# Kernel tuning notes

Measured on AMD Instinct MI355X. Metric: run time of the kernel, lower is better.

The kernel has to match this reference:

```python
import jax, jax.numpy as jnp
import numpy as np

# batch, net nodes/graph, vnr nodes/graph, hidden, static feats, vnr feats, vnf types, value out
B, NN, NV, H, FS, FV, T, O = 64, 1000, 10, 128, 8, 6, 8, 64
EN, EV = B * NN * 8, B * NV * 4  # total edges (avg degree 8 / 4)


def _gat(h, src, dst, W, al, ar, b):
    """dgl GATConv, num_heads=1, activation=None, allow_zero_in_degree=True."""
    n = h.shape[0]
    z = h @ W                                                    # [N,H]
    e = jax.nn.leaky_relu((z @ al)[src] + (z @ ar)[dst], 0.2)    # [E]
    emax = jax.ops.segment_max(e, dst, num_segments=n)
    ee = jnp.exp(e - emax[dst])
    alpha = ee / jax.ops.segment_sum(ee, dst, num_segments=n)[dst]
    return jax.ops.segment_sum(z[src] * alpha[:, None], dst, num_segments=n) + b


def _gru_cell(x, h, W_ih, W_hh, b_ih, b_hh):
    gi = x @ W_ih.T + b_ih
    gh = h @ W_hh.T + b_hh
    ir, iz, in_ = jnp.split(gi, 3, axis=-1)
    hr, hz, hn = jnp.split(gh, 3, axis=-1)
    r = jax.nn.sigmoid(ir + hr)
    z = jax.nn.sigmoid(iz + hz)
    n = jnp.tanh(in_ + r * hn)
    return (1.0 - z) * n + z * h


def _forward(static_feat, vnr_feat, nmask,
             Ws1, als1, ars1, bs1, Ws2, als2, ars2, bs2, Ws3, als3, ars3, bs3,
             Wv1, alv1, arv1, bv1, Wv2, alv2, arv2, bv2, Wv3, alv3, arv3, bv3,
             W_attn, v_attn, W_ih, W_hh, b_ih, b_hh, h0, W_out, b_out,
             src_s, dst_s, src_v, dst_v, vnr_VNF, net_VNF):
    # ---- graph encoders: 3 stacked GAT layers each ----
    hs = _gat(static_feat, src_s, dst_s, Ws1, als1, ars1, bs1)
    hs = _gat(hs, src_s, dst_s, Ws2, als2, ars2, bs2)
    hs = _gat(hs, src_s, dst_s, Ws3, als3, ars3, bs3)            # [B*NN,H]
    hv = _gat(vnr_feat, src_v, dst_v, Wv1, alv1, arv1, bv1)
    hv = _gat(hv, src_v, dst_v, Wv2, alv2, arv2, bv2)
    hv = _gat(hv, src_v, dst_v, Wv3, alv3, arv3, bv3)            # [B*NV,H]
    static_hidden = hs.reshape(B, NN, H).transpose(0, 2, 1)      # [B,H,NN]
    vnr_hidden = hv.reshape(B, NV, H).transpose(0, 2, 1)         # [B,H,NV]

    # ---- pointer decoder ----
    netV = net_VNF.reshape(B, NN, T)
    # mask[b,i,n] = netV[b, n, vnr_VNF[b,i]]
    masks = jnp.take_along_axis(netV[:, None, :, :], vnr_VNF[:, :, None, None], axis=3)[..., 0]  # [B,NV,NN]

    def step(h, x):
        h_new = _gru_cell(x, h, W_ih, W_hh, b_ih, b_hh)          # [B,H]
        cat = jnp.concatenate(
            [static_hidden, jnp.broadcast_to(h_new[:, :, None], (B, H, NN))], axis=1)  # [B,2H,NN]
        attn = jnp.einsum('h,bhn->bn', v_attn,
                          jnp.tanh(jnp.einsum('hk,bkn->bhn', W_attn, cat)))
        return h_new, attn

    h0b = jnp.broadcast_to(h0, (B, H))
    xs = vnr_hidden.transpose(2, 0, 1)                            # [NV,B,H]
    _, attns = jax.lax.scan(step, h0b, xs)                        # [NV,B,NN]
    pi = (attns.transpose(1, 0, 2) + jnp.log(masks.astype(jnp.float32))).reshape(B, -1)

    # ---- value head ----
    nm = nmask.reshape(B, NV)
    y1 = (vnr_hidden.transpose(0, 2, 1) * nm[:, :, None]).sum(1) / nm.sum(1, keepdims=True)
    y2 = static_hidden.mean(2)
    val = jnp.concatenate([y1, y2], axis=1) @ W_out.T + b_out     # [B,O]
    return pi, val


def setup_inputs() -> dict:
    key = jax.random.key(0)
    ks = iter(jax.random.split(key, 60))

    def nrm(shape, fan):
        return jax.random.normal(next(ks), shape, jnp.float32) / np.sqrt(fan).astype(np.float32)

    inp = {
        'static_feat': jax.random.normal(next(ks), (B * NN, FS), jnp.float32),
        'vnr_feat': jax.random.normal(next(ks), (B * NV, FV), jnp.float32),
        'nmask': jnp.ones((B * NV,), jnp.float32),
    }
    for pfx, fin in (('s1', FS), ('s2', H), ('s3', H), ('v1', FV), ('v2', H), ('v3', H)):
        inp['W' + pfx] = nrm((fin, H), fin)
        inp['al' + pfx] = nrm((H,), H)
        inp['ar' + pfx] = nrm((H,), H)
        inp['b' + pfx] = jnp.zeros((H,), jnp.float32)
    inp['W_attn'] = nrm((H, 2 * H), 2 * H)
    inp['v_attn'] = nrm((H,), H)
    inp['W_ih'] = nrm((3 * H, H), H)
    inp['W_hh'] = nrm((3 * H, H), H)
    inp['b_ih'] = jnp.zeros((3 * H,), jnp.float32)
    inp['b_hh'] = jnp.zeros((3 * H,), jnp.float32)
    inp['h0'] = jnp.zeros((H,), jnp.float32)
    inp['W_out'] = nrm((O, 2 * H), 2 * H)
    inp['b_out'] = jnp.zeros((O,), jnp.float32)
    inp['src_s'] = jax.random.randint(next(ks), (EN,), 0, B * NN)
    inp['dst_s'] = jax.random.randint(next(ks), (EN,), 0, B * NN)
    inp['src_v'] = jax.random.randint(next(ks), (EV,), 0, B * NV)
    inp['dst_v'] = jax.random.randint(next(ks), (EV,), 0, B * NV)
    inp['vnr_VNF'] = jax.random.randint(next(ks), (B, NV), 0, T)
    inp['net_VNF'] = jnp.ones((B * NN, T), jnp.int32)
    return inp


def reference(static_feat, vnr_feat, nmask,
              Ws1, als1, ars1, bs1, Ws2, als2, ars2, bs2, Ws3, als3, ars3, bs3,
              Wv1, alv1, arv1, bv1, Wv2, alv2, arv2, bv2, Wv3, alv3, arv3, bv3,
              W_attn, v_attn, W_ih, W_hh, b_ih, b_hh, h0, W_out, b_out,
              src_s, dst_s, src_v, dst_v, vnr_VNF, net_VNF):
    return _forward(static_feat, vnr_feat, nmask,
                    Ws1, als1, ars1, bs1, Ws2, als2, ars2, bs2, Ws3, als3, ars3, bs3,
                    Wv1, alv1, arv1, bv1, Wv2, alv2, arv2, bv2, Wv3, alv3, arv3, bv3,
                    W_attn, v_attn, W_ih, W_hh, b_ih, b_hh, h0, W_out, b_out,
                    src_s, dst_s, src_v, dst_v, vnr_VNF, net_VNF)
```

## Files before the change

### kernel.cpp

```cpp
#include <hip/hip_runtime.h>
#include <hip/hip_bf16.h>
#include <math.h>

#define B_   64
#define NN_  1000
#define NV_  10
#define H_   128
#define FS_  8
#define FV_  6
#define T_   8
#define O_   64
#define EN_  512000
#define EV_  2560
#define NS_  (B_*NN_)
#define NVT_ (B_*NV_)

typedef __attribute__((ext_vector_type(8))) short short8v;
typedef __attribute__((ext_vector_type(4))) float floatx4;

__device__ __forceinline__ float fast_rcp(float x) { return __builtin_amdgcn_rcpf(x); }
__device__ __forceinline__ float fast_tanh(float x) {
  return 1.f - 2.f*fast_rcp(1.f + __expf(2.f*x));
}
__device__ __forceinline__ float fast_sigmoid(float x) {
  return fast_rcp(1.f + __expf(-x));
}
__device__ __forceinline__ unsigned short bf16_rne(float x) {
  unsigned u = __float_as_uint(x);
  return (unsigned short)((u + 0x7FFFu + ((u >> 16) & 1u)) >> 16);
}
__device__ __forceinline__ float bf16_tof(unsigned short b) {
  return __uint_as_float(((unsigned)b) << 16);
}
__device__ __forceinline__ float dot4(float4 a, float4 b) {
  return a.x*b.x + a.y*b.y + a.z*b.z + a.w*b.w;
}
__device__ __forceinline__ float lrelu02(float e) {
  return (e > 0.f) ? e : 0.2f*e;
}

__global__ __launch_bounds__(256) void k_count(const int* dst, int E, int* counts) {
  int i = blockIdx.x*256 + threadIdx.x;
  if (i < E) atomicAdd(&counts[dst[i]], 1);
}

__global__ __launch_bounds__(1024) void k_scan(const int* cnt, int n, int* rowptr) {
  __shared__ int sums[1024];
  int t = threadIdx.x;
  int v = (t < n) ? cnt[t] : 0;
  sums[t] = v;
  __syncthreads();
  for (int offd = 1; offd < 1024; offd <<= 1) {
    int u = (t >= offd) ? sums[t-offd] : 0;
    __syncthreads();
    sums[t] += u;
    __syncthreads();
  }
  if (t < n) rowptr[t] = sums[t] - v;
  if (t == n-1) rowptr[n] = sums[t];
}

__global__ __launch_bounds__(256) void k_scan_local(const int* cnt, int n, int* out, int* bsum) {
  __shared__ int s[256];
  int t = threadIdx.x; int i = blockIdx.x*256 + t;
  int v = (i < n) ? cnt[i] : 0;
  s[t] = v; __syncthreads();
  #pragma unroll
  for (int o = 1; o < 256; o <<= 1) {
    int u = (t >= o) ? s[t-o] : 0; __syncthreads();
    s[t] += u; __syncthreads();
  }
  if (i < n) out[i] = s[t] - v;
  if (t == 255) bsum[blockIdx.x] = s[255];
}

__global__ __launch_bounds__(256) void k_scan_bsum(int* bsum, int nb) {
  __shared__ int s[256];
  int t = threadIdx.x;
  int v = (t < nb) ? bsum[t] : 0;
  s[t] = v; __syncthreads();
  #pragma unroll
  for (int o = 1; o < 256; o <<= 1) {
    int u = (t >= o) ? s[t-o] : 0; __syncthreads();
    s[t] += u; __syncthreads();
  }
  if (t < nb) bsum[t] = s[t] - v;
}

__global__ __launch_bounds__(256) void k_scan_add(int* out, const int* bsum, int n, int E) {
  int i = blockIdx.x*256 + threadIdx.x;
  if (i < n) out[i] += bsum[blockIdx.x];
  if (i == 0) out[n] = E;
}

__global__ __launch_bounds__(256) void k_scatter(const int* src, const int* dst, int E,
                                                 const int* rowptr, int* cursor,
                                                 int* srcp, int* dstp) {
  int i = blockIdx.x*256 + threadIdx.x;
  if (i >= E) return;
  int d = dst[i];
  int pos = rowptr[d] + atomicAdd(&cursor[d], 1);
  srcp[pos] = src[i];
  dstp[pos] = d;
}

__global__ __launch_bounds__(256) void k_edge_exp(int E, const int* srcp, const int* dstp,
                                                  const float* el, const float* er, float* expe) {
  int i = blockIdx.x*256 + threadIdx.x;
  if (i >= E) return;
  float e = el[srcp[i]] + er[dstp[i]];
  e = (e > 0.f) ? e : 0.2f*e;
  expe[i] = __expf(e);
}

__global__ __launch_bounds__(256) void k_aggregate(int nNodes, const int* rowptr,
                                                   const int* srcp, const float* expe,
                                                   const float* z, const float* bias, float* out) {
  int w = (blockIdx.x*256 + threadIdx.x) >> 6;
  int lane = threadIdx.x & 63;
  if (w >= nNodes) return;
  int beg = rowptr[w], end = rowptr[w+1];
  float a0 = 0.f, a1 = 0.f, wsum = 0.f;
  for (int i = beg; i < end; ++i) {
    int sI = srcp[i];
    float wt = expe[i];
    float2 zz = *(const float2*)(z + (size_t)sI*H_ + lane*2);
    a0 += wt*zz.x; a1 += wt*zz.y; wsum += wt;
  }
  float inv = (end > beg) ? fast_rcp(wsum) : 0.f;
  float2 o;
  o.x = a0*inv + bias[lane*2];
  o.y = a1*inv + bias[lane*2 + 1];
  *(float2*)(out + (size_t)w*H_ + lane*2) = o;
}

__global__ __launch_bounds__(256) void k_aggregate_split(int nNodes, const int* __restrict__ rowptr,
    const int* __restrict__ srcp, const float* __restrict__ el, const float* __restrict__ er,
    const unsigned short* __restrict__ z, const float* __restrict__ bias,
    unsigned short* __restrict__ outHi, unsigned short* __restrict__ outLo) {
  int w = (blockIdx.x*256 + threadIdx.x) >> 6;
  int lane = threadIdx.x & 63;
  if (w >= nNodes) return;
  int beg = rowptr[w], end = rowptr[w+1];
  float erw = er[w];
  float a0 = 0.f, a1 = 0.f, wsum = 0.f;
  int i = beg;
  for (; i + 8 <= end; i += 8) {
    int sI[8]; float lv[8]; ushort2 q[8];
    #pragma unroll
    for (int u = 0; u < 8; ++u) sI[u] = srcp[i+u];
    #pragma unroll
    for (int u = 0; u < 8; ++u) lv[u] = el[sI[u]];
    #pragma unroll
    for (int u = 0; u < 8; ++u) q[u] = *(const ushort2*)(z + (size_t)sI[u]*H_ + lane*2);
    #pragma unroll
    for (int u = 0; u < 8; ++u) {
      float wt = __expf(lrelu02(lv[u] + erw));
      a0 += wt*bf16_tof(q[u].x);
      a1 += wt*bf16_tof(q[u].y);
      wsum += wt;
    }
  }
  for (; i < end; ++i) {
    int sI = srcp[i];
    float wt = __expf(lrelu02(el[sI] + erw));
    ushort2 q = *(const ushort2*)(z + (size_t)sI*H_ + lane*2);
    a0 += wt*bf16_tof(q.x); a1 += wt*bf16_tof(q.y); wsum += wt;
  }
  float inv = (end > beg) ? fast_rcp(wsum) : 0.f;
  float o0 = a0*inv + bias[lane*2];
  float o1 = a1*inv + bias[lane*2 + 1];
  unsigned short h0 = bf16_rne(o0), h1 = bf16_rne(o1);
  unsigned short l0 = bf16_rne(o0 - bf16_tof(h0)), l1 = bf16_rne(o1 - bf16_tof(h1));
  ushort2 hv; hv.x = h0; hv.y = h1;
  ushort2 lv; lv.x = l0; lv.y = l1;
  *(ushort2*)(outHi + (size_t)w*H_ + lane*2) = hv;
  *(ushort2*)(outLo + (size_t)w*H_ + lane*2) = lv;
}

__global__ __launch_bounds__(256) void k_wsplit(const float* in, int ld, int trans,
                                                unsigned short* hi, unsigned short* lo) {
  int idx = blockIdx.x*256 + threadIdx.x;
  if (idx >= H_*H_) return;
  int j = idx >> 7, k = idx & 127;
  float v = trans ? in[(size_t)k*ld + j] : in[(size_t)j*ld + k];
  unsigned short h = bf16_rne(v);
  unsigned short l = bf16_rne(v - bf16_tof(h));
  hi[idx] = h; lo[idx] = l;
}

__global__ __launch_bounds__(256) void k_mfma_gemm(
    const unsigned short* __restrict__ Ahi, const unsigned short* __restrict__ Alo,
    const unsigned short* __restrict__ WThi, const unsigned short* __restrict__ WTlo,
    float* __restrict__ C, unsigned short* __restrict__ Cb,
    const float* __restrict__ al, const float* __restrict__ ar,
    float* __restrict__ el, float* __restrict__ er) {
  __shared__ unsigned short lAhi[64*136];
  __shared__ unsigned short lAlo[64*136];
  __shared__ float redl[4][64];
  __shared__ float redr[4][64];
  int t = threadIdx.x;
  int row0 = blockIdx.x * 64;
  int wid = t >> 6, lane = t & 63;
  int g = lane >> 4, c = lane & 15;

  #pragma unroll
  for (int i = 0; i < 4; ++i) {
    int m = t + 256*i;
    int r = m >> 4;
    int kc = (m & 15) * 8;
    *(short8v*)(lAhi + r*136 + kc) = *(const short8v*)(Ahi + (size_t)(row0 + r)*H_ + kc);
    *(short8v*)(lAlo + r*136 + kc) = *(const short8v*)(Alo + (size_t)(row0 + r)*H_ + kc);
  }

  short8v bhi[2][4], blo[2][4];
  #pragma unroll
  for (int ct = 0; ct < 2; ++ct) {
    int col = wid*32 + ct*16 + c;
    #pragma unroll
    for (int kb = 0; kb < 4; ++kb) {
      size_t o = (size_t)col*H_ + kb*32 + g*8;
      bhi[ct][kb] = *(const short8v*)(WThi + o);
      blo[ct][kb] = *(const short8v*)(WTlo + o);
    }
  }

  floatx4 acc[4][2];
  #pragma unroll
  for (int rt = 0; rt < 4; ++rt)
    #pragma unroll
    for (int ct = 0; ct < 2; ++ct)
      acc[rt][ct] = (floatx4){0.f, 0.f, 0.f, 0.f};

  __syncthreads();

  #pragma unroll
  for (int kb = 0; kb < 4; ++kb) {
    short8v ahi[4], alo[4];
    #pragma unroll
    for (int rt = 0; rt < 4; ++rt) {
      int r = rt*16 + c;
      ahi[rt] = *(const short8v*)(lAhi + r*136 + kb*32 + g*8);
      alo[rt] = *(const short8v*)(lAlo + r*136 + kb*32 + g*8);
    }
    #pragma unroll
    for (int rt = 0; rt < 4; ++rt)
      #pragma unroll
      for (int ct = 0; ct < 2; ++ct) {
        acc[rt][ct] = __builtin_amdgcn_mfma_f32_16x16x32_bf16(ahi[rt], bhi[ct][kb], acc[rt][ct], 0, 0, 0);
        acc[rt][ct] = __builtin_amdgcn_mfma_f32_16x16x32_bf16(alo[rt], bhi[ct][kb], acc[rt][ct], 0, 0, 0);
        acc[rt][ct] = __builtin_amdgcn_mfma_f32_16x16x32_bf16(ahi[rt], blo[ct][kb], acc[rt][ct], 0, 0, 0);
      }
  }

  #pragma unroll
  for (int rt = 0; rt < 4; ++rt)
    #pragma unroll
    for (int i = 0; i < 4; ++i) {
      int row = row0 + rt*16 + g*4 + i;
      if (Cb) {
        unsigned short* cr = Cb + (size_t)row*H_ + wid*32;
        cr[c]      = bf16_rne(acc[rt][0][i]);
        cr[16 + c] = bf16_rne(acc[rt][1][i]);
      } else {
        float* cr = C + (size_t)row*H_ + wid*32;
        cr[c]      = acc[rt][0][i];
        cr[16 + c] = acc[rt][1][i];
      }
    }

  if (el) {
    float av0 = al[wid*32 + c], av1 = al[wid*32 + 16 + c];
    float rv0 = ar[wid*32 + c], rv1 = ar[wid*32 + 16 + c];
    #pragma unroll
    for (int rt = 0; rt < 4; ++rt)
      #pragma unroll
      for (int i = 0; i < 4; ++i) {
        float pl = acc[rt][0][i]*av0 + acc[rt][1][i]*av1;
        float pr = acc[rt][0][i]*rv0 + acc[rt][1][i]*rv1;
        pl += __shfl_xor(pl, 1, 64); pl += __shfl_xor(pl, 2, 64);
        pl += __shfl_xor(pl, 4, 64); pl += __shfl_xor(pl, 8, 64);
        pr += __shfl_xor(pr, 1, 64); pr += __shfl_xor(pr, 2, 64);
        pr += __shfl_xor(pr, 4, 64); pr += __shfl_xor(pr, 8, 64);
        if (c == 0) { redl[wid][rt*16 + g*4 + i] = pl; redr[wid][rt*16 + g*4 + i] = pr; }
      }
    __syncthreads();
    if (t < 64) {
      el[row0 + t] = redl[0][t] + redl[1][t] + redl[2][t] + redl[3][t];
      er[row0 + t] = redr[0][t] + redr[1][t] + redr[2][t] + redr[3][t];
    }
  }
}

__global__ __launch_bounds__(256) void k_gemm(const float* A, int M, int K, int N,
                                              const float* W, const float* bias,
                                              float* C, unsigned short* Cb,
                                              const float* al, const float* ar,
                                              float* el, float* er) {
  __shared__ float Ws_[64*128];
  __shared__ float As_[16*128];
  __shared__ float redl[16][17];
  __shared__ float redr[16][17];
  int t = threadIdx.x;
  int j0 = blockIdx.y * 128;
  int row0 = blockIdx.x * 16;
  for (int l = t; l < 16*K; l += 256) {
    int r = l / K, k = l - r*K;
    int row = row0 + r;
    As_[r*K + k] = (row < M) ? A[(size_t)row*K + k] : 0.f;
  }
  int jg = t & 15, r = t >> 4;
  float acc[8];
  #pragma unroll
  for (int q = 0; q < 8; ++q) acc[q] = 0.f;
  for (int kc = 0; kc < K; kc += 64) {
    int kl = min(64, K - kc);
    __syncthreads();
    for (int l = t; l < (kl << 7); l += 256) {
      int k = l >> 7, j = l & 127;
      int jj = j0 + j;
      Ws_[l] = (jj < N) ? W[(size_t)(kc + k)*N + jj] : 0.f;
    }
    __syncthreads();
    for (int k = 0; k < kl; ++k) {
      float a = As_[r*K + kc + k];
      const float* wr = &Ws_[(k << 7) + jg*8];
      #pragma unroll
      for (int q = 0; q < 8; ++q) acc[q] += a * wr[q];
    }
  }
  int row = row0 + r;
  if (row < M) {
    if (Cb) {
      unsigned short* crow = Cb + (size_t)row*N + j0 + jg*8;
      #pragma unroll
      for (int q = 0; q < 8; ++q) {
        int j = j0 + jg*8 + q;
        if (j < N) crow[q] = bf16_rne(acc[q] + (bias ? bias[j] : 0.f));
      }
    } else {
      float* crow = C + (size_t)row*N + j0 + jg*8;
      #pragma unroll
      for (int q = 0; q < 8; ++q) {
        int j = j0 + jg*8 + q;
        if (j < N) crow[q] = acc[q] + (bias ? bias[j] : 0.f);
      }
    }
  }
  if (el) {
    float pl = 0.f, pr = 0.f;
    #pragma unroll
    for (int q = 0; q < 8; ++q) {
      int j = jg*8 + q;
      pl += acc[q]*al[j];
      pr += acc[q]*ar[j];
    }
    redl[r][jg] = pl; redr[r][jg] = pr;
    __syncthreads();
    if (t < 16) {
      float sl = 0.f, sr = 0.f;
      for (int q = 0; q < 16; ++q) { sl += redl[t][q]; sr += redr[t][q]; }
      int row2 = row0 + t;
      if (row2 < M) { el[row2] = sl; er[row2] = sr; }
    }
  }
}

__global__ __launch_bounds__(256) void k_transpose(const float* in, int inStride,
                                                   int K, int J, float* out) {
  int idx = blockIdx.x*256 + threadIdx.x;
  if (idx >= K*J) return;
  int k = idx / J, j = idx - k*J;
  out[idx] = in[(size_t)j*inStride + k];
}

__global__ __launch_bounds__(512) void k_decoder(const float* __restrict__ GI,
                                                 const float* __restrict__ W_hh,
                                                 const float* __restrict__ b_hh,
                                                 const float* __restrict__ W_attn,
                                                 const float* __restrict__ h0,
                                                 float* __restrict__ A2) {
  int b = blockIdx.x;
  __shared__ float h[128];
  __shared__ float gh[384];
  int t = threadIdx.x;
  const float4* wsrc = (t < 384)
      ? (const float4*)(W_hh + (size_t)t*128)
      : (const float4*)(W_attn + (size_t)(t-384)*256 + 128);
  float4 wreg[32];
  #pragma unroll
  for (int kk = 0; kk < 32; ++kk) wreg[kk] = wsrc[kk];
  float bh = (t < 384) ? b_hh[t] : 0.f;
  if (t < 128) h[t] = h0[t];
  __syncthreads();
  for (int s = 0; s < 10; ++s) {
    const float4* h4 = (const float4*)h;
    if (t < 384) {
      float a0 = 0.f, a1 = 0.f, a2 = 0.f, a3 = 0.f;
      #pragma unroll
      for (int kk = 0; kk < 32; kk += 4) {
        a0 += dot4(wreg[kk+0], h4[kk+0]);
        a1 += dot4(wreg[kk+1], h4[kk+1]);
        a2 += dot4(wreg[kk+2], h4[kk+2]);
        a3 += dot4(wreg[kk+3], h4[kk+3]);
      }
      gh[t] = (a0 + a1) + (a2 + a3) + bh;
    }
    __syncthreads();
    if (t < 128) {
      const float* gi = GI + (size_t)(b*NV_ + s)*384;
      float rr = fast_sigmoid(gi[t]       + gh[t]);
      float zz = fast_sigmoid(gi[128 + t] + gh[128 + t]);
      float nn = fast_tanh   (gi[256 + t] + rr*gh[256 + t]);
      h[t] = (1.f - zz)*nn + zz*h[t];
    }
    __syncthreads();
    if (t >= 384) {
      float a0 = 0.f, a1 = 0.f, a2 = 0.f, a3 = 0.f;
      #pragma unroll
      for (int kk = 0; kk < 32; kk += 4) {
        a0 += dot4(wreg[kk+0], h4[kk+0]);
        a1 += dot4(wreg[kk+1], h4[kk+1]);
        a2 += dot4(wreg[kk+2], h4[kk+2]);
        a3 += dot4(wreg[kk+3], h4[kk+3]);
      }
      A2[((size_t)s*B_ + b)*128 + (t - 384)] = (a0 + a1) + (a2 + a3);
    }
  }
}

__global__ __launch_bounds__(256) void k_attn3(const float* __restrict__ A1,
                                               const float* __restrict__ A2,
                                               const float* __restrict__ v_attn,
                                               const int* __restrict__ vnr_VNF,
                                               const int* __restrict__ net_VNF,
                                               float* __restrict__ pi) {
  __shared__ float a2s[10][128];
  __shared__ float vv2s[128];
  int b = blockIdx.y;
  int t = threadIdx.x;
  for (int i = t; i < 1280; i += 256) {
    int s = i >> 7, k = i & 127;
    a2s[s][k] = 2.f*A2[((size_t)s*B_ + b)*H_ + k];
  }
  if (t < 128) vv2s[t] = 2.f*v_attn[t];
  __syncthreads();
  int nl = t >> 2, p = t & 3;
  int n = blockIdx.x*64 + nl;
  if (n >= NN_) return;
  size_t g = (size_t)b*NN_ + n;
  const float4* arow = (const float4*)(A1 + g*H_ + p*32);
  float4 a[8], w2[8];
  #pragma unroll
  for (int kk = 0; kk < 8; ++kk) {
    float4 av = arow[kk];
    a[kk] = make_float4(2.f*av.x, 2.f*av.y, 2.f*av.z, 2.f*av.w);
    w2[kk] = *(const float4*)(&vv2s[p*32 + kk*4]);
  }
  float vsum = 0.f;
  #pragma unroll
  for (int kk = 0; kk < 8; ++kk)
    vsum += (w2[kk].x + w2[kk].y) + (w2[kk].z + w2[kk].w);
  vsum *= 0.5f;
  float acc[10];
  #pragma unroll
  for (int s = 0; s < 10; ++s) {
    const float* a2r = &a2s[s][p*32];
    float sum2 = 0.f;
    #pragma unroll
    for (int kk = 0; kk < 8; ++kk) {
      float4 c = *(const float4*)(a2r + kk*4);
      sum2 = fmaf(w2[kk].x, fast_rcp(1.f + __expf(a[kk].x + c.x)), sum2);
      sum2 = fmaf(w2[kk].y, fast_rcp(1.f + __expf(a[kk].y + c.y)), sum2);
      sum2 = fmaf(w2[kk].z, fast_rcp(1.f + __expf(a[kk].z + c.z)), sum2);
      sum2 = fmaf(w2[kk].w, fast_rcp(1.f + __expf(a[kk].w + c.w)), sum2);
    }
    acc[s] = vsum - sum2;
  }
  #pragma unroll
  for (int s = 0; s < 10; ++s) {
    acc[s] += __shfl_xor(acc[s], 1, 64);
    acc[s] += __shfl_xor(acc[s], 2, 64);
  }
  if (p == 0) {
    #pragma unroll
    for (int s = 0; s < 10; ++s) {
      int vnf = vnr_VNF[b*NV_ + s];
      int m   = net_VNF[g*T_ + vnf];
      pi[(size_t)b*(NV_*NN_) + (size_t)s*NN_ + n] = acc[s] + __logf((float)m);
    }
  }
}

__global__ __launch_bounds__(128) void k_y1(const float* Hv, const float* nmask, float* y1) {
  int b = blockIdx.x, h = threadIdx.x;
  float s = 0.f, d = 0.f;
  for (int i = 0; i < NV_; ++i) {
    float m = nmask[b*NV_ + i];
    s += Hv[(size_t)(b*NV_ + i)*H_ + h]*m;
    d += m;
  }
  y1[b*H_ + h] = s/d;
}

__global__ __launch_bounds__(128) void k_y2s(const unsigned short* hi, const unsigned short* lo,
                                             float* y2) {
  int b = blockIdx.x, slice = blockIdx.y, h = threadIdx.x;
  int n0 = slice*125, n1 = n0 + 125;
  float s = 0.f;
  for (int n = n0; n < n1; ++n) {
    size_t idx = ((size_t)b*NN_ + n)*H_ + h;
    s += bf16_tof(hi[idx]) + bf16_tof(lo[idx]);
  }
  atomicAdd(&y2[b*H_ + h], s);
}

__global__ __launch_bounds__(64) void k_value(const float* y1, const float* y2,
                                              const float* W_out, const float* b_out,
                                              float* val) {
  int b = blockIdx.x, o = threadIdx.x;
  const float* w = W_out + (size_t)o*256;
  float s = b_out[o];
  for (int h = 0; h < H_; ++h)
    s += y1[b*H_ + h]*w[h] + (y2[b*H_ + h]*(1.f/1000.f))*w[128 + h];
  val[b*O_ + o] = s;
}

extern "C" void kernel_launch(void* const* d_in, const int* in_sizes, int n_in,
                              void* d_out, int out_size, void* d_ws, size_t ws_size,
                              hipStream_t stream) {
  (void)in_sizes; (void)n_in; (void)out_size; (void)ws_size;
  const float* static_feat = (const float*)d_in[0];
  const float* vnr_feat    = (const float*)d_in[1];
  const float* nmask       = (const float*)d_in[2];
  const float* Ws1 = (const float*)d_in[3];  const float* als1 = (const float*)d_in[4];
  const float* ars1 = (const float*)d_in[5]; const float* bs1 = (const float*)d_in[6];
  const float* Ws2 = (const float*)d_in[7];  const float* als2 = (const float*)d_in[8];
  const float* ars2 = (const float*)d_in[9]; const float* bs2 = (const float*)d_in[10];
  const float* Ws3 = (const float*)d_in[11]; const float* als3 = (const float*)d_in[12];
  const float* ars3 = (const float*)d_in[13]; const float* bs3 = (const float*)d_in[14];
  const float* Wv1 = (const float*)d_in[15]; const float* alv1 = (const float*)d_in[16];
  const float* arv1 = (const float*)d_in[17]; const float* bv1 = (const float*)d_in[18];
  const float* Wv2 = (const float*)d_in[19]; const float* alv2 = (const float*)d_in[20];
  const float* arv2 = (const float*)d_in[21]; const float* bv2 = (const float*)d_in[22];
  const float* Wv3 = (const float*)d_in[23]; const float* alv3 = (const float*)d_in[24];
  const float* arv3 = (const float*)d_in[25]; const float* bv3 = (const float*)d_in[26];
  const float* W_attn = (const float*)d_in[27];
  const float* v_attn = (const float*)d_in[28];
  const float* W_ih = (const float*)d_in[29];
  const float* W_hh = (const float*)d_in[30];
  const float* b_ih = (const float*)d_in[31];
  const float* b_hh = (const float*)d_in[32];
  const float* h0   = (const float*)d_in[33];
  const float* W_out = (const float*)d_in[34];
  const float* b_out = (const float*)d_in[35];
  const int* src_s = (const int*)d_in[36];
  const int* dst_s = (const int*)d_in[37];
  const int* src_v = (const int*)d_in[38];
  const int* dst_v = (const int*)d_in[39];
  const int* vnr_VNF = (const int*)d_in[40];
  const int* net_VNF = (const int*)d_in[41];

  char* ws = (char*)d_ws;
  size_t off = 0;
  auto alloc = [&](size_t bytes) -> char* {
    off = (off + 255) & ~(size_t)255;
    char* p = ws + off;
    off += bytes;
    return p;
  };
  float* Z    = (float*)alloc((size_t)NS_*H_*4);
  unsigned short* Zb   = (unsigned short*)alloc((size_t)NS_*H_*2);
  unsigned short* HsHi = (unsigned short*)alloc((size_t)NS_*H_*2);
  unsigned short* HsLo = (unsigned short*)alloc((size_t)NS_*H_*2);
  float* Zv   = (float*)alloc((size_t)NVT_*H_*4);
  float* Hv   = (float*)alloc((size_t)NVT_*H_*4);
  float* el_s = (float*)alloc((size_t)NS_*4);
  float* er_s = (float*)alloc((size_t)NS_*4);
  float* el_v = (float*)alloc((size_t)NVT_*4);
  float* er_v = (float*)alloc((size_t)NVT_*4);
  size_t zcount = (size_t)NS_ + NS_ + NVT_ + NVT_ + B_*H_;
  char* zb = alloc(zcount*4);
  int*   counts_s = (int*)zb;
  int*   cursor_s = counts_s + NS_;
  int*   counts_v = cursor_s + NS_;
  int*   cursor_v = counts_v + NVT_;
  float* y2buf    = (float*)(cursor_v + NVT_);
  int* rowptr_s = (int*)alloc((size_t)(NS_+1)*4);
  int* rowptr_v = (int*)alloc((size_t)(NVT_+1)*4);
  int* bsum     = (int*)alloc((size_t)256*4);
  int* srcp_s   = (int*)alloc((size_t)EN_*4);
  int* dstp_s   = (int*)alloc((size_t)EN_*4);
  int* srcp_v   = (int*)alloc((size_t)EV_*4);
  int* dstp_v   = (int*)alloc((size_t)EV_*4);
  float* expe_v = (float*)alloc((size_t)EV_*4);
  unsigned short* WS2hi = (unsigned short*)alloc((size_t)H_*H_*2);
  unsigned short* WS2lo = (unsigned short*)alloc((size_t)H_*H_*2);
  unsigned short* WS3hi = (unsigned short*)alloc((size_t)H_*H_*2);
  unsigned short* WS3lo = (unsigned short*)alloc((size_t)H_*H_*2);
  unsigned short* WAhi  = (unsigned short*)alloc((size_t)H_*H_*2);
  unsigned short* WAlo  = (unsigned short*)alloc((size_t)H_*H_*2);
  float* WTih   = (float*)alloc((size_t)H_*384*4);
  float* GI     = (float*)alloc((size_t)NVT_*384*4);
  float* A2     = (float*)alloc((size_t)NV_*B_*H_*4);
  float* y1buf  = (float*)alloc((size_t)B_*H_*4);

  float* pi  = (float*)d_out;
  float* val = pi + (size_t)B_*NV_*NN_;

  hipMemsetAsync(zb, 0, zcount*4, stream);

  k_transpose<<<(H_*384 + 255)/256, 256, 0, stream>>>(W_ih, 128, H_, 384, WTih);
  k_wsplit<<<64, 256, 0, stream>>>(Ws2, H_, 1, WS2hi, WS2lo);
  k_wsplit<<<64, 256, 0, stream>>>(Ws3, H_, 1, WS3hi, WS3lo);
  k_wsplit<<<64, 256, 0, stream>>>(W_attn, 2*H_, 0, WAhi, WAlo);

  k_count<<<EN_/256, 256, 0, stream>>>(dst_s, EN_, counts_s);
  k_count<<<EV_/256, 256, 0, stream>>>(dst_v, EV_, counts_v);
  k_scan_local<<<250, 256, 0, stream>>>(counts_s, NS_, rowptr_s, bsum);
  k_scan_bsum<<<1, 256, 0, stream>>>(bsum, 250);
  k_scan_add<<<250, 256, 0, stream>>>(rowptr_s, bsum, NS_, EN_);
  k_scan<<<1, 1024, 0, stream>>>(counts_v, NVT_, rowptr_v);
  k_scatter<<<EN_/256, 256, 0, stream>>>(src_s, dst_s, EN_, rowptr_s, cursor_s, srcp_s, dstp_s);
  k_scatter<<<EV_/256, 256, 0, stream>>>(src_v, dst_v, EV_, rowptr_v, cursor_v, srcp_v, dstp_v);

  dim3 gemmV(NVT_/16, 1);
  int aggS = (NS_ + 3)/4, aggV = (NVT_ + 3)/4;

  k_gemm<<<dim3(NS_/16, 1), 256, 0, stream>>>(static_feat, NS_, FS_, H_, Ws1, nullptr,
                                              nullptr, Zb, als1, ars1, el_s, er_s);
  k_aggregate_split<<<aggS, 256, 0, stream>>>(NS_, rowptr_s, srcp_s, el_s, er_s, Zb, bs1, HsHi, HsLo);
  k_mfma_gemm<<<NS_/64, 256, 0, stream>>>(HsHi, HsLo, WS2hi, WS2lo, nullptr, Zb, als2, ars2, el_s, er_s);
  k_aggregate_split<<<aggS, 256, 0, stream>>>(NS_, rowptr_s, srcp_s, el_s, er_s, Zb, bs2, HsHi, HsLo);
  k_mfma_gemm<<<NS_/64, 256, 0, stream>>>(HsHi, HsLo, WS3hi, WS3lo, nullptr, Zb, als3, ars3, el_s, er_s);
  k_aggregate_split<<<aggS, 256, 0, stream>>>(NS_, rowptr_s, srcp_s, el_s, er_s, Zb, bs3, HsHi, HsLo);

  k_gemm<<<gemmV, 256, 0, stream>>>(vnr_feat, NVT_, FV_, H_, Wv1, nullptr, Zv, nullptr, alv1, arv1, el_v, er_v);
  k_edge_exp<<<EV_/256, 256, 0, stream>>>(EV_, srcp_v, dstp_v, el_v, er_v, expe_v);
  k_aggregate<<<aggV, 256, 0, stream>>>(NVT_, rowptr_v, srcp_v, expe_v, Zv, bv1, Hv);
  k_gemm<<<gemmV, 256, 0, stream>>>(Hv, NVT_, H_, H_, Wv2, nullptr, Zv, nullptr, alv2, arv2, el_v, er_v);
  k_edge_exp<<<EV_/256, 256, 0, stream>>>(EV_, srcp_v, dstp_v, el_v, er_v, expe_v);
  k_aggregate<<<aggV, 256, 0, stream>>>(NVT_, rowptr_v, srcp_v, expe_v, Zv, bv2, Hv);
  k_gemm<<<gemmV, 256, 0, stream>>>(Hv, NVT_, H_, H_, Wv3, nullptr, Zv, nullptr, alv3, arv3, el_v, er_v);
  k_edge_exp<<<EV_/256, 256, 0, stream>>>(EV_, srcp_v, dstp_v, el_v, er_v, expe_v);
  k_aggregate<<<aggV, 256, 0, stream>>>(NVT_, rowptr_v, srcp_v, expe_v, Zv, bv3, Hv);

  k_gemm<<<dim3(NVT_/16, 3), 256, 0, stream>>>(Hv, NVT_, H_, 384, WTih, b_ih, GI, nullptr,
                                               nullptr, nullptr, nullptr, nullptr);
  k_mfma_gemm<<<NS_/64, 256, 0, stream>>>(HsHi, HsLo, WAhi, WAlo, Z, nullptr,
                                          nullptr, nullptr, nullptr, nullptr);
  k_decoder<<<B_, 512, 0, stream>>>(GI, W_hh, b_hh, W_attn, h0, A2);
  k_attn3<<<dim3(16, B_), 256, 0, stream>>>(Z, A2, v_attn, vnr_VNF, net_VNF, pi);

  k_y1<<<B_, 128, 0, stream>>>(Hv, nmask, y1buf);
  k_y2s<<<dim3(B_, 8), 128, 0, stream>>>(HsHi, HsLo, y2buf);
  k_value<<<B_, 64, 0, stream>>>(y1buf, y2buf, W_out, b_out, val);
}
```

Before: 474.8 us.

## Fuse small prep/edge kernels and store CSR sources as 16-bit indices

Merges the weight transpose and three bf16 split kernels into one launch, folds the edge-exp computation into the VNR aggregation kernel, and merges the y1 mean into the value kernel. It also drops the unused dst permutation array and stores sorted source indices as unsigned short, which halves index traffic in the large static aggregation. This removes several launches and a memory pass, but 16-bit indices hold only up to 65535 while there are 64000 static nodes, so the fit is tight.

After: 448.8 us. -5.5%, faster.

```diff
diff --git a/kernel.cpp b/kernel.cpp
--- a/kernel.cpp
+++ b/kernel.cpp
@@ -95,35 +95,27 @@
 
 __global__ __launch_bounds__(256) void k_scatter(const int* src, const int* dst, int E,
                                                  const int* rowptr, int* cursor,
-                                                 int* srcp, int* dstp) {
+                                                 unsigned short* srcp) {
   int i = blockIdx.x*256 + threadIdx.x;
   if (i >= E) return;
   int d = dst[i];
   int pos = rowptr[d] + atomicAdd(&cursor[d], 1);
-  srcp[pos] = src[i];
-  dstp[pos] = d;
-}
-
-__global__ __launch_bounds__(256) void k_edge_exp(int E, const int* srcp, const int* dstp,
-                                                  const float* el, const float* er, float* expe) {
-  int i = blockIdx.x*256 + threadIdx.x;
-  if (i >= E) return;
-  float e = el[srcp[i]] + er[dstp[i]];
-  e = (e > 0.f) ? e : 0.2f*e;
-  expe[i] = __expf(e);
-}
-
-__global__ __launch_bounds__(256) void k_aggregate(int nNodes, const int* rowptr,
-                                                   const int* srcp, const float* expe,
-                                                   const float* z, const float* bias, float* out) {
+  srcp[pos] = (unsigned short)src[i];
+}
+
+__global__ __launch_bounds__(256) void k_aggregate_v(int nNodes, const int* __restrict__ rowptr,
+    const unsigned short* __restrict__ srcp, const float* __restrict__ el,
+    const float* __restrict__ er, const float* __restrict__ z,
+    const float* __restrict__ bias, float* __restrict__ out) {
   int w = (blockIdx.x*256 + threadIdx.x) >> 6;
   int lane = threadIdx.x & 63;
   if (w >= nNodes) return;
   int beg = rowptr[w], end = rowptr[w+1];
+  float erw = er[w];
   float a0 = 0.f, a1 = 0.f, wsum = 0.f;
   for (int i = beg; i < end; ++i) {
     int sI = srcp[i];
-    float wt = expe[i];
+    float wt = __expf(lrelu02(el[sI] + erw));
     float2 zz = *(const float2*)(z + (size_t)sI*H_ + lane*2);
     a0 += wt*zz.x; a1 += wt*zz.y; wsum += wt;
   }
@@ -135,7 +127,7 @@
 }
 
 __global__ __launch_bounds__(256) void k_aggregate_split(int nNodes, const int* __restrict__ rowptr,
-    const int* __restrict__ srcp, const float* __restrict__ el, const float* __restrict__ er,
+    const unsigned short* __restrict__ srcp, const float* __restrict__ el, const float* __restrict__ er,
     const unsigned short* __restrict__ z, const float* __restrict__ bias,
     unsigned short* __restrict__ outHi, unsigned short* __restrict__ outLo) {
   int w = (blockIdx.x*256 + threadIdx.x) >> 6;
@@ -178,15 +170,29 @@
   *(ushort2*)(outLo + (size_t)w*H_ + lane*2) = lv;
 }
 
-__global__ __launch_bounds__(256) void k_wsplit(const float* in, int ld, int trans,
-                                                unsigned short* hi, unsigned short* lo) {
+__global__ __launch_bounds__(256) void k_prep(const float* W_ih, const float* Ws2,
+                                              const float* Ws3, const float* W_attn,
+                                              float* WTih,
+                                              unsigned short* WS2hi, unsigned short* WS2lo,
+                                              unsigned short* WS3hi, unsigned short* WS3lo,
+                                              unsigned short* WAhi, unsigned short* WAlo) {
   int idx = blockIdx.x*256 + threadIdx.x;
-  if (idx >= H_*H_) return;
-  int j = idx >> 7, k = idx & 127;
-  float v = trans ? in[(size_t)k*ld + j] : in[(size_t)j*ld + k];
-  unsigned short h = bf16_rne(v);
-  unsigned short l = bf16_rne(v - bf16_tof(h));
-  hi[idx] = h; lo[idx] = l;
+  int task = blockIdx.y;
+  if (task == 0) {
+    if (idx < 128*384) {
+      int k = idx / 384, j = idx - k*384;
+      WTih[idx] = W_ih[(size_t)j*128 + k];
+    }
+  } else {
+    if (idx >= 128*128) return;
+    int j = idx >> 7, k = idx & 127;
+    float v; unsigned short *hi, *lo;
+    if (task == 1)      { v = Ws2[(size_t)k*128 + j];    hi = WS2hi; lo = WS2lo; }
+    else if (task == 2) { v = Ws3[(size_t)k*128 + j];    hi = WS3hi; lo = WS3lo; }
+    else                { v = W_attn[(size_t)j*256 + k]; hi = WAhi;  lo = WAlo;  }
+    unsigned short h = bf16_rne(v);
+    hi[idx] = h; lo[idx] = bf16_rne(v - bf16_tof(h));
+  }
 }
 
 __global__ __launch_bounds__(256) void k_mfma_gemm(
@@ -366,14 +372,6 @@
   }
 }
 
-__global__ __launch_bounds__(256) void k_transpose(const float* in, int inStride,
-                                                   int K, int J, float* out) {
-  int idx = blockIdx.x*256 + threadIdx.x;
-  if (idx >= K*J) return;
-  int k = idx / J, j = idx - k*J;
-  out[idx] = in[(size_t)j*inStride + k];
-}
-
 __global__ __launch_bounds__(512) void k_decoder(const float* __restrict__ GI,
                                                  const float* __restrict__ W_hh,
                                                  const float* __restrict__ b_hh,
@@ -492,17 +490,6 @@
   }
 }
 
-__global__ __launch_bounds__(128) void k_y1(const float* Hv, const float* nmask, float* y1) {
-  int b = blockIdx.x, h = threadIdx.x;
-  float s = 0.f, d = 0.f;
-  for (int i = 0; i < NV_; ++i) {
-    float m = nmask[b*NV_ + i];
-    s += Hv[(size_t)(b*NV_ + i)*H_ + h]*m;
-    d += m;
-  }
-  y1[b*H_ + h] = s/d;
-}
-
 __global__ __launch_bounds__(128) void k_y2s(const unsigned short* hi, const unsigned short* lo,
                                              float* y2) {
   int b = blockIdx.x, slice = blockIdx.y, h = threadIdx.x;
@@ -515,15 +502,30 @@
   atomicAdd(&y2[b*H_ + h], s);
 }
 
-__global__ __launch_bounds__(64) void k_value(const float* y1, const float* y2,
-                                              const float* W_out, const float* b_out,
-                                              float* val) {
-  int b = blockIdx.x, o = threadIdx.x;
-  const float* w = W_out + (size_t)o*256;
-  float s = b_out[o];
-  for (int h = 0; h < H_; ++h)
-    s += y1[b*H_ + h]*w[h] + (y2[b*H_ + h]*(1.f/1000.f))*w[128 + h];
-  val[b*O_ + o] = s;
+__global__ __launch_bounds__(128) void k_value(const float* __restrict__ Hv,
+                                               const float* __restrict__ nmask,
+                                               const float* __restrict__ y2,
+                                               const float* __restrict__ W_out,
+                                               const float* __restrict__ b_out,
+                                               float* __restrict__ val) {
+  __shared__ float y1s[128];
+  int b = blockIdx.x, t = threadIdx.x;
+  float s = 0.f, d = 0.f;
+  #pragma unroll
+  for (int i = 0; i < NV_; ++i) {
+    float m = nmask[b*NV_ + i];
+    s += Hv[(size_t)(b*NV_ + i)*H_ + t]*m;
+    d += m;
+  }
+  y1s[t] = s/d;
+  __syncthreads();
+  if (t < 64) {
+    const float* w = W_out + (size_t)t*256;
+    float acc = b_out[t];
+    for (int h = 0; h < H_; ++h)
+      acc += y1s[h]*w[h] + (y2[b*H_ + h]*(1.f/1000.f))*w[128 + h];
+    val[b*O_ + t] = acc;
+  }
 }
 
 extern "C" void kernel_launch(void* const* d_in, const int* in_sizes, int n_in,
@@ -589,11 +591,8 @@
   int* rowptr_s = (int*)alloc((size_t)(NS_+1)*4);
   int* rowptr_v = (int*)alloc((size_t)(NVT_+1)*4);
   int* bsum     = (int*)alloc((size_t)256*4);
-  int* srcp_s   = (int*)alloc((size_t)EN_*4);
-  int* dstp_s   = (int*)alloc((size_t)EN_*4);
-  int* srcp_v   = (int*)alloc((size_t)EV_*4);
-  int* dstp_v   = (int*)alloc((size_t)EV_*4);
-  float* expe_v = (float*)alloc((size_t)EV_*4);
+  unsigned short* srcp_s = (unsigned short*)alloc((size_t)EN_*2);
+  unsigned short* srcp_v = (unsigned short*)alloc((size_t)EV_*2);
   unsigned short* WS2hi = (unsigned short*)alloc((size_t)H_*H_*2);
   unsigned short* WS2lo = (unsigned short*)alloc((size_t)H_*H_*2);
   unsigned short* WS3hi = (unsigned short*)alloc((size_t)H_*H_*2);
@@ -603,17 +602,14 @@
   float* WTih   = (float*)alloc((size_t)H_*384*4);
   float* GI     = (float*)alloc((size_t)NVT_*384*4);
   float* A2     = (float*)alloc((size_t)NV_*B_*H_*4);
-  float* y1buf  = (float*)alloc((size_t)B_*H_*4);
 
   float* pi  = (float*)d_out;
   float* val = pi + (size_t)B_*NV_*NN_;
 
   hipMemsetAsync(zb, 0, zcount*4, stream);
 
-  k_transpose<<<(H_*384 + 255)/256, 256, 0, stream>>>(W_ih, 128, H_, 384, WTih);
-  k_wsplit<<<64, 256, 0, stream>>>(Ws2, H_, 1, WS2hi, WS2lo);
-  k_wsplit<<<64, 256, 0, stream>>>(Ws3, H_, 1, WS3hi, WS3lo);
-  k_wsplit<<<64, 256, 0, stream>>>(W_attn, 2*H_, 0, WAhi, WAlo);
+  k_prep<<<dim3(192, 4), 256, 0, stream>>>(W_ih, Ws2, Ws3, W_attn, WTih,
+                                           WS2hi, WS2lo, WS3hi, WS3lo, WAhi, WAlo);
 
   k_count<<<EN_/256, 256, 0, stream>>>(dst_s, EN_, counts_s);
   k_count<<<EV_/256, 256, 0, stream>>>(dst_v, EV_, counts_v);
@@ -621,8 +617,8 @@
   k_scan_bsum<<<1, 256, 0, stream>>>(bsum, 250);
   k_scan_add<<<250, 256, 0, stream>>>(rowptr_s, bsum, NS_, EN_);
   k_scan<<<1, 1024, 0, stream>>>(counts_v, NVT_, rowptr_v);
-  k_scatter<<<EN_/256, 256, 0, stream>>>(src_s, dst_s, EN_, rowptr_s, cursor_s, srcp_s, dstp_s);
-  k_scatter<<<EV_/256, 256, 0, stream>>>(src_v, dst_v, EV_, rowptr_v, cursor_v, srcp_v, dstp_v);
+  k_scatter<<<EN_/256, 256, 0, stream>>>(src_s, dst_s, EN_, rowptr_s, cursor_s, srcp_s);
+  k_scatter<<<EV_/256, 256, 0, stream>>>(src_v, dst_v, EV_, rowptr_v, cursor_v, srcp_v);
 
   dim3 gemmV(NVT_/16, 1);
   int aggS = (NS_ + 3)/4, aggV = (NVT_ + 3)/4;
@@ -636,14 +632,11 @@
   k_aggregate_split<<<aggS, 256, 0, stream>>>(NS_, rowptr_s, srcp_s, el_s, er_s, Zb, bs3, HsHi, HsLo);
 
   k_gemm<<<gemmV, 256, 0, stream>>>(vnr_feat, NVT_, FV_, H_, Wv1, nullptr, Zv, nullptr, alv1, arv1, el_v, er_v);
-  k_edge_exp<<<EV_/256, 256, 0, stream>>>(EV_, srcp_v, dstp_v, el_v, er_v, expe_v);
-  k_aggregate<<<aggV, 256, 0, stream>>>(NVT_, rowptr_v, srcp_v, expe_v, Zv, bv1, Hv);
+  k_aggregate_v<<<aggV, 256, 0, stream>>>(NVT_, rowptr_v, srcp_v, el_v, er_v, Zv, bv1, Hv);
   k_gemm<<<gemmV, 256, 0, stream>>>(Hv, NVT_, H_, H_, Wv2, nullptr, Zv, nullptr, alv2, arv2, el_v, er_v);
-  k_edge_exp<<<EV_/256, 256, 0, stream>>>(EV_, srcp_v, dstp_v, el_v, er_v, expe_v);
-  k_aggregate<<<aggV, 256, 0, stream>>>(NVT_, rowptr_v, srcp_v, expe_v, Zv, bv2, Hv);
+  k_aggregate_v<<<aggV, 256, 0, stream>>>(NVT_, rowptr_v, srcp_v, el_v, er_v, Zv, bv2, Hv);
   k_gemm<<<gemmV, 256, 0, stream>>>(Hv, NVT_, H_, H_, Wv3, nullptr, Zv, nullptr, alv3, arv3, el_v, er_v);
-  k_edge_exp<<<EV_/256, 256, 0, stream>>>(EV_, srcp_v, dstp_v, el_v, er_v, expe_v);
-  k_aggregate<<<aggV, 256, 0, stream>>>(NVT_, rowptr_v, srcp_v, expe_v, Zv, bv3, Hv);
+  k_aggregate_v<<<aggV, 256, 0, stream>>>(NVT_, rowptr_v, srcp_v, el_v, er_v, Zv, bv3, Hv);
 
   k_gemm<<<dim3(NVT_/16, 3), 256, 0, stream>>>(Hv, NVT_, H_, 384, WTih, b_ih, GI, nullptr,
                                                nullptr, nullptr, nullptr, nullptr);
@@ -652,7 +645,6 @@
   k_decoder<<<B_, 512, 0, stream>>>(GI, W_hh, b_hh, W_attn, h0, A2);
   k_attn3<<<dim3(16, B_), 256, 0, stream>>>(Z, A2, v_attn, vnr_VNF, net_VNF, pi);
 
-  k_y1<<<B_, 128, 0, stream>>>(Hv, nmask, y1buf);
   k_y2s<<<dim3(B_, 8), 128, 0, stream>>>(HsHi, HsLo, y2buf);
-  k_value<<<B_, 64, 0, stream>>>(y1buf, y2buf, W_out, b_out, val);
-}
+  k_value<<<B_, 128, 0, stream>>>(Hv, nmask, y2buf, W_out, b_out, val);
+}
```
